# Performance work log

Hardware: AMD Instinct MI355X
Metric: run time of the kernel (lower is better)

## Reference

```python
import jax, jax.numpy as jnp
import numpy as np

# Mamba dims: d_model=1024, expand=2 -> d_inner=2048, d_state=16, d_conv=4, dt_rank=ceil(1024/16)=64
B, L, D = 2, 1024, 1024
DIN, N, R, K = 2048, 16, 64, 4
LN_EPS = 1e-5


def setup_inputs():
    key = jax.random.key(0)
    ks = jax.random.split(key, 12)
    s = lambda fan_in: 1.0 / np.sqrt(fan_in)
    inp = {
        "x": jax.random.normal(ks[0], (B, L, D), jnp.float32),
        "W_in": jax.random.normal(ks[1], (D, 2 * DIN), jnp.float32) * s(D),
        "conv_w": jax.random.normal(ks[2], (DIN, K), jnp.float32) * s(K),
        "conv_b": jax.random.normal(ks[3], (DIN,), jnp.float32) * 0.02,
        "W_x": jax.random.normal(ks[4], (DIN, R + 2 * N), jnp.float32) * s(DIN),
        "W_dt": jax.random.normal(ks[5], (R, DIN), jnp.float32) * s(R),
        # bias chosen so softplus(bias) ~ small positive dt
        "b_dt": jnp.full((DIN,), -4.0, jnp.float32)
        + jax.random.normal(ks[6], (DIN,), jnp.float32) * 0.1,
        # S4D-real init: A = -[1..N] broadcast over channels
        "A_log": jnp.log(jnp.broadcast_to(jnp.arange(1, N + 1, dtype=jnp.float32), (DIN, N))),
        "D_skip": jnp.ones((DIN,), jnp.float32),
        "W_out": jax.random.normal(ks[7], (DIN, D), jnp.float32) * s(DIN),
        "ln_g": jnp.ones((D,), jnp.float32),
        "ln_b": jnp.zeros((D,), jnp.float32),
    }
    return inp


def _silu(x):
    return x * jax.nn.sigmoid(x)


def _mamba_forward(x, W_in, conv_w, conv_b, W_x, W_dt, b_dt, A_log, D_skip, W_out, ln_g, ln_b):
    # in_proj -> (x_in, z), each [B, L, DIN]
    xz = jnp.einsum("bld,de->ble", x, W_in)
    x_in, z = jnp.split(xz, 2, axis=-1)

    # causal depthwise conv1d (kernel K=4) via shifted sums
    xp = jnp.pad(x_in, ((0, 0), (K - 1, 0), (0, 0)))  # [B, L+K-1, DIN]
    x_conv = conv_b
    for k in range(K):
        x_conv = x_conv + xp[:, k : k + L, :] * conv_w[:, k]
    x_conv = _silu(x_conv)  # [B, L, DIN]

    # x_proj -> dt_rank + 2*N
    x_dbl = jnp.einsum("bld,de->ble", x_conv, W_x)
    dt, Bc, Cc = jnp.split(x_dbl, [R, R + N], axis=-1)  # [B,L,R], [B,L,N], [B,L,N]
    delta = jax.nn.softplus(jnp.einsum("blr,rd->bld", dt, W_dt) + b_dt)  # [B,L,DIN]

    A = -jnp.exp(A_log)  # [DIN, N]
    # discretize: deltaA [B,L,DIN,N], deltaB_u [B,L,DIN,N]
    deltaA = jnp.exp(delta[..., None] * A)
    deltaBu = delta[..., None] * Bc[:, :, None, :] * x_conv[..., None]

    # selective scan over time
    def step(h, inp):
        dA, dBu, C_t = inp  # [B,DIN,N], [B,DIN,N], [B,N]
        h = dA * h + dBu
        y_t = jnp.einsum("bdn,bn->bd", h, C_t)
        return h, y_t

    h0 = jnp.zeros((B, DIN, N), jnp.float32)
    xs = (
        jnp.moveaxis(deltaA, 1, 0),
        jnp.moveaxis(deltaBu, 1, 0),
        jnp.moveaxis(Cc, 1, 0),
    )
    _, ys = jax.lax.scan(step, h0, xs)  # ys: [L, B, DIN]
    y = jnp.moveaxis(ys, 0, 1) + x_conv * D_skip  # [B, L, DIN]

    y = y * _silu(z)
    out = jnp.einsum("bld,de->ble", y, W_out)  # [B, L, D]

    # post LayerNorm
    mu = jnp.mean(out, axis=-1, keepdims=True)
    var = jnp.mean(jnp.square(out - mu), axis=-1, keepdims=True)
    return (out - mu) * jax.lax.rsqrt(var + LN_EPS) * ln_g + ln_b


def reference(x, W_in, conv_w, conv_b, W_x, W_dt, b_dt, A_log, D_skip, W_out, ln_g, ln_b):
    return _mamba_forward(x, W_in, conv_w, conv_b, W_x, W_dt, b_dt, A_log, D_skip, W_out, ln_g, ln_b)
```

## Files before the change

kernel.cpp:

```cpp
#include <hip/hip_runtime.h>

#define LSEQ 1024
#define DMODEL 1024
#define DINNER 2048
#define NSTATE 16
#define RRANK 64
#define CHUNK 32
#define NCHUNK 32
#define KSPLIT 8

typedef unsigned short u16;
typedef __attribute__((ext_vector_type(8))) short bf16x8;
typedef __attribute__((ext_vector_type(4))) short bf16x4;
typedef __attribute__((ext_vector_type(4))) float f32x4;

__device__ __forceinline__ float sigmoidf_(float x) {
    return 1.0f / (1.0f + __expf(-x));
}
__device__ __forceinline__ float softplusf_(float x) {
    return (x > 20.0f) ? x : log1pf(__expf(x));
}
__device__ __forceinline__ short f2bf(float f) {
    union { float f; unsigned u; } v; v.f = f;
    unsigned r = v.u + 0x7FFF + ((v.u >> 16) & 1);
    return (short)(r >> 16);
}
__device__ __forceinline__ float bf2f(u16 b) {
    union { unsigned u; float f; } v; v.u = ((unsigned)b) << 16;
    return v.f;
}
__device__ __forceinline__ void async_cp16(const u16* g, u16* l) {
    __builtin_amdgcn_global_load_lds(
        (const __attribute__((address_space(1))) unsigned int*)g,
        (__attribute__((address_space(3))) unsigned int*)l, 16, 0, 0);
}

__global__ __launch_bounds__(256) void cast_bf16_kernel(
    const float* __restrict__ in, u16* __restrict__ out)
{
    const size_t i = ((size_t)blockIdx.x * 256 + threadIdx.x) * 8;
    float4 a = *(const float4*)&in[i];
    float4 b = *(const float4*)&in[i + 4];
    bf16x8 o;
    o[0] = f2bf(a.x); o[1] = f2bf(a.y); o[2] = f2bf(a.z); o[3] = f2bf(a.w);
    o[4] = f2bf(b.x); o[5] = f2bf(b.y); o[6] = f2bf(b.z); o[7] = f2bf(b.w);
    *(bf16x8*)&out[i] = o;
}

__global__ __launch_bounds__(256) void transpose_cast2_kernel(
    const float* __restrict__ in0, u16* __restrict__ out0,
    const float* __restrict__ in1, u16* __restrict__ out1)
{
    __shared__ float t[32][33];
    int bid = blockIdx.x;
    const float* in; u16* out; int R, C, bxi, byi;
    if (bid < 4096) { in = in0; out = out0; R = DMODEL;  C = 2 * DINNER; bxi = bid & 127; byi = bid >> 7; }
    else { bid -= 4096; in = in1; out = out1; R = DINNER; C = DMODEL;    bxi = bid & 31;  byi = bid >> 5; }
    const int bx = bxi * 32, by = byi * 32;
    const int tx = threadIdx.x & 31, ty = threadIdx.x >> 5;
    #pragma unroll
    for (int i = 0; i < 4; ++i)
        t[ty + 8 * i][tx] = in[(size_t)(by + ty + 8 * i) * C + bx + tx];
    __syncthreads();
    #pragma unroll
    for (int i = 0; i < 4; ++i)
        out[(size_t)(bx + ty + 8 * i) * R + by + tx] = (u16)f2bf(t[tx][ty + 8 * i]);
}

template<int BM, int BN, bool BSPLIT>
__global__ __launch_bounds__(256) void mfma_gemm_kernel(
    const u16* __restrict__ A, const u16* __restrict__ Bt,
    float* __restrict__ C0, u16* __restrict__ C1,
    int M, int N, int K, int Nsplit)
{
    constexpr int WMS = BM / 32;
    constexpr int WNS = BN / 32;
    __shared__ u16 lA[BM * 32];
    __shared__ u16 lB[BN * 32];

    const int tid  = threadIdx.x;
    const int lane = tid & 63, wave = tid >> 6;
    const int quad = lane >> 4, l16 = lane & 15;
    const int wm   = (wave >> 1) * (BM / 2);
    const int wn   = (wave & 1) * (BN / 2);
    const int row0 = blockIdx.y * BM;
    const int col0 = blockIdx.x * BN;

    f32x4 acc[WMS][WNS];
    #pragma unroll
    for (int i = 0; i < WMS; ++i)
        #pragma unroll
        for (int j = 0; j < WNS; ++j)
            acc[i][j] = (f32x4){0.f, 0.f, 0.f, 0.f};

    for (int k0 = 0; k0 < K; k0 += 32) {
        #pragma unroll
        for (int t = 0; t < BM / 64; ++t) {
            int c = tid + t * 256;
            int r = c >> 2, kc = c & 3;
            async_cp16(&A[(size_t)(row0 + r) * K + k0 + kc * 8], &lA[c * 8]);
        }
        #pragma unroll
        for (int t = 0; t < BN / 64; ++t) {
            int c = tid + t * 256;
            int r = c >> 2, kc = c & 3;
            async_cp16(&Bt[(size_t)(col0 + r) * K + k0 + kc * 8], &lB[c * 8]);
        }
        __syncthreads();
        bf16x8 af[WMS], bfr[WNS];
        #pragma unroll
        for (int i = 0; i < WMS; ++i)
            af[i] = *(bf16x8*)&lA[(wm + i * 16 + l16) * 32 + quad * 8];
        #pragma unroll
        for (int j = 0; j < WNS; ++j)
            bfr[j] = *(bf16x8*)&lB[(wn + j * 16 + l16) * 32 + quad * 8];
        #pragma unroll
        for (int i = 0; i < WMS; ++i)
            #pragma unroll
            for (int j = 0; j < WNS; ++j)
                acc[i][j] = __builtin_amdgcn_mfma_f32_16x16x32_bf16(
                    af[i], bfr[j], acc[i][j], 0, 0, 0);
        __syncthreads();
    }
    if (!BSPLIT || col0 < Nsplit) {
        const int ldc = BSPLIT ? Nsplit : N;
        #pragma unroll
        for (int i = 0; i < WMS; ++i)
            #pragma unroll
            for (int j = 0; j < WNS; ++j)
                #pragma unroll
                for (int r = 0; r < 4; ++r)
                    C0[(size_t)(row0 + wm + i * 16 + quad * 4 + r) * ldc
                       + col0 + wn + j * 16 + l16] = acc[i][j][r];
    } else {
        const int ldc = N - Nsplit, ccol = col0 - Nsplit;
        #pragma unroll
        for (int i = 0; i < WMS; ++i)
            #pragma unroll
            for (int j = 0; j < WNS; ++j)
                #pragma unroll
                for (int r = 0; r < 4; ++r)
                    C1[(size_t)(row0 + wm + i * 16 + quad * 4 + r) * ldc
                       + ccol + wn + j * 16 + l16] = (u16)f2bf(acc[i][j][r]);
    }
}

__global__ __launch_bounds__(256) void conv_silu_kernel(
    const float* __restrict__ X1, const float* __restrict__ cw,
    const float* __restrict__ cb, u16* __restrict__ xcb)
{
    const int idx = blockIdx.x * 256 + threadIdx.x;
    const int dq  = idx % (DINNER / 4);
    const int bl  = idx / (DINNER / 4);
    const int l   = bl % LSEQ;
    const int d0  = dq * 4;

    const float4* cw4 = (const float4*)cw;
    const float4 W0 = cw4[d0 + 0];
    const float4 W1 = cw4[d0 + 1];
    const float4 W2 = cw4[d0 + 2];
    const float4 W3 = cw4[d0 + 3];
    float4 s = *(const float4*)&cb[d0];

    #pragma unroll
    for (int k = 0; k < 4; ++k) {
        int ls = l + k - 3;
        if (ls >= 0) {
            float4 xv = *(const float4*)&X1[(size_t)(bl + k - 3) * DINNER + d0];
            s.x = fmaf(xv.x, ((const float*)&W0)[k], s.x);
            s.y = fmaf(xv.y, ((const float*)&W1)[k], s.y);
            s.z = fmaf(xv.z, ((const float*)&W2)[k], s.z);
            s.w = fmaf(xv.w, ((const float*)&W3)[k], s.w);
        }
    }
    bf16x4 o;
    o[0] = f2bf(s.x * sigmoidf_(s.x));
    o[1] = f2bf(s.y * sigmoidf_(s.y));
    o[2] = f2bf(s.z * sigmoidf_(s.z));
    o[3] = f2bf(s.w * sigmoidf_(s.w));
    *(bf16x4*)&xcb[(size_t)idx * 4] = o;
}

__global__ __launch_bounds__(256) void xproj_part_kernel(
    const u16* __restrict__ xcb, const float* __restrict__ Wx,
    float* __restrict__ part)
{
    __shared__ float As[32][64 + 4];
    __shared__ float Ws[32][96 + 4];

    const int tid  = threadIdx.x;
    const int tx   = tid % 32;
    const int ty   = tid / 32;
    const int row0 = blockIdx.x * 64;
    const int k0   = blockIdx.y * (DINNER / KSPLIT);

    float acc[8][3];
    #pragma unroll
    for (int i = 0; i < 8; ++i) { acc[i][0] = 0.f; acc[i][1] = 0.f; acc[i][2] = 0.f; }

    for (int kt = 0; kt < DINNER / KSPLIT; kt += 32) {
        const int kb = k0 + kt;
        {
            int m = tid >> 2, kq = tid & 3;
            bf16x8 v = *(const bf16x8*)&xcb[(size_t)(row0 + m) * DINNER + kb + kq * 8];
            #pragma unroll
            for (int j = 0; j < 8; ++j)
                As[kq * 8 + j][m] = bf2f((u16)v[j]);
        }
        #pragma unroll
        for (int i = 0; i < 3; ++i) {
            int lin = tid + i * 256;
            int kk = lin / 24, q = lin % 24;
            *(float4*)&Ws[kk][q * 4] = *(const float4*)&Wx[(size_t)(kb + kk) * 96 + q * 4];
        }
        __syncthreads();
        #pragma unroll 8
        for (int kk = 0; kk < 32; ++kk) {
            float a[8];
            *(float4*)&a[0] = *(const float4*)&As[kk][ty * 8];
            *(float4*)&a[4] = *(const float4*)&As[kk][ty * 8 + 4];
            float b0 = Ws[kk][tx], b1 = Ws[kk][tx + 32], b2 = Ws[kk][tx + 64];
            #pragma unroll
            for (int i = 0; i < 8; ++i) {
                acc[i][0] = fmaf(a[i], b0, acc[i][0]);
                acc[i][1] = fmaf(a[i], b1, acc[i][1]);
                acc[i][2] = fmaf(a[i], b2, acc[i][2]);
            }
        }
        __syncthreads();
    }
    float* po = part + (size_t)blockIdx.y * (2 * LSEQ * 96);
    #pragma unroll
    for (int i = 0; i < 8; ++i) {
        int r = row0 + ty * 8 + i;
        po[(size_t)r * 96 + tx]      = acc[i][0];
        po[(size_t)r * 96 + tx + 32] = acc[i][1];
        po[(size_t)r * 96 + tx + 64] = acc[i][2];
    }
}

__global__ __launch_bounds__(256) void xproj_reduce_kernel(
    const float* __restrict__ part, float* __restrict__ xdbl)
{
    const int idx = blockIdx.x * 256 + threadIdx.x;
    float s = 0.0f;
    #pragma unroll
    for (int k = 0; k < KSPLIT; ++k)
        s += part[(size_t)k * (2 * LSEQ * 96) + idx];
    xdbl[idx] = s;
}

__global__ __launch_bounds__(256) void delta_kernel(
    const float* __restrict__ xdbl, const float* __restrict__ Wdt,
    const float* __restrict__ bdt, u16* __restrict__ deltab)
{
    __shared__ float As[64][64 + 4];
    __shared__ float Ws[64][64 + 4];
    const int tid  = threadIdx.x;
    const int tx   = tid % 16;
    const int ty   = tid / 16;
    const int row0 = blockIdx.y * 64;
    const int col0 = blockIdx.x * 64;

    #pragma unroll
    for (int i = 0; i < 4; ++i) {
        int lin = tid + i * 256;
        int m = lin / 16, kq = lin % 16;
        float4 v = *(const float4*)&xdbl[(size_t)(row0 + m) * 96 + kq * 4];
        As[kq * 4 + 0][m] = v.x;
        As[kq * 4 + 1][m] = v.y;
        As[kq * 4 + 2][m] = v.z;
        As[kq * 4 + 3][m] = v.w;
    }
    #pragma unroll
    for (int i = 0; i < 4; ++i) {
        int lin = tid + i * 256;
        int kk = lin / 16, q = lin % 16;
        *(float4*)&Ws[kk][q * 4] = *(const float4*)&Wdt[(size_t)kk * DINNER + col0 + q * 4];
    }
    __syncthreads();

    float acc[4][4];
    #pragma unroll
    for (int i = 0; i < 4; ++i)
        #pragma unroll
        for (int j = 0; j < 4; ++j) acc[i][j] = 0.0f;

    #pragma unroll 8
    for (int kk = 0; kk < 64; ++kk) {
        float4 a = *(const float4*)&As[kk][ty * 4];
        float4 b = *(const float4*)&Ws[kk][tx * 4];
        const float* ap = (const float*)&a;
        const float* bp = (const float*)&b;
        #pragma unroll
        for (int i = 0; i < 4; ++i)
            #pragma unroll
            for (int j = 0; j < 4; ++j)
                acc[i][j] = fmaf(ap[i], bp[j], acc[i][j]);
    }

    float4 bv = *(const float4*)&bdt[col0 + tx * 4];
    const float* bvp = (const float*)&bv;
    #pragma unroll
    for (int i = 0; i < 4; ++i) {
        bf16x4 o;
        o[0] = f2bf(softplusf_(acc[i][0] + bvp[0]));
        o[1] = f2bf(softplusf_(acc[i][1] + bvp[1]));
        o[2] = f2bf(softplusf_(acc[i][2] + bvp[2]));
        o[3] = f2bf(softplusf_(acc[i][3] + bvp[3]));
        *(bf16x4*)&deltab[(size_t)(row0 + ty * 4 + i) * DINNER + col0 + tx * 4] = o;
    }
}

__global__ __launch_bounds__(256) void scan_part1_kernel(
    const u16* __restrict__ deltab, const u16* __restrict__ xcb,
    const float* __restrict__ xdbl, const float* __restrict__ A_log,
    float* __restrict__ Pbuf, float* __restrict__ Hbuf)
{
    const int d  = blockIdx.x * 256 + threadIdx.x;
    const int b  = blockIdx.y;
    const int ch = blockIdx.z;

    float Aa[NSTATE];
    #pragma unroll
    for (int q = 0; q < 4; ++q) {
        float4 v = *(const float4*)&A_log[(size_t)d * NSTATE + q * 4];
        Aa[q * 4 + 0] = -__expf(v.x);
        Aa[q * 4 + 1] = -__expf(v.y);
        Aa[q * 4 + 2] = -__expf(v.z);
        Aa[q * 4 + 3] = -__expf(v.w);
    }
    float h[NSTATE], P[NSTATE];
    #pragma unroll
    for (int n = 0; n < NSTATE; ++n) { h[n] = 0.0f; P[n] = 1.0f; }

    const size_t row0 = (size_t)b * LSEQ + (size_t)ch * CHUNK;
    #pragma unroll 4
    for (int t = 0; t < CHUNK; ++t) {
        const size_t row = row0 + t;
        float dv  = bf2f(deltab[row * DINNER + d]);
        float xcv = bf2f(xcb[row * DINNER + d]);
        float du  = dv * xcv;
        const float4* br = (const float4*)&xdbl[row * 96 + RRANK];
        float4 B4[4] = { br[0], br[1], br[2], br[3] };
        const float* Bv = (const float*)B4;
        #pragma unroll
        for (int n = 0; n < NSTATE; ++n) {
            float dA = __expf(dv * Aa[n]);
            h[n] = fmaf(dA, h[n], du * Bv[n]);
            P[n] *= dA;
        }
    }
    float* Pp = &Pbuf[(((size_t)ch * 2 + b) * DINNER + d) * NSTATE];
    float* Hp = &Hbuf[(((size_t)ch * 2 + b) * DINNER + d) * NSTATE];
    #pragma unroll
    for (int q = 0; q < 4; ++q) {
        *(float4*)&Pp[q * 4] = *(float4*)&P[q * 4];
        *(float4*)&Hp[q * 4] = *(float4*)&h[q * 4];
    }
}

__global__ __launch_bounds__(256) void scan_combine_kernel(
    const float* __restrict__ Pbuf, const float* __restrict__ Hbuf,
    float* __restrict__ h0buf)
{
    const int idx = blockIdx.x * 256 + threadIdx.x;
    float H = 0.0f;
    #pragma unroll 8
    for (int cch = 0; cch < NCHUNK; ++cch) {
        const size_t g = (size_t)cch * (2 * DINNER * NSTATE) + idx;
        h0buf[g] = H;
        H = fmaf(Pbuf[g], H, Hbuf[g]);
    }
}

__global__ __launch_bounds__(256) void scan_part2_kernel(
    const u16* __restrict__ deltab, const u16* __restrict__ xcb,
    const float* __restrict__ xdbl, const float* __restrict__ h0buf,
    const u16* __restrict__ Zb, u16* __restrict__ yb,
    const float* __restrict__ A_log, const float* __restrict__ Dskip)
{
    const int d  = blockIdx.x * 256 + threadIdx.x;
    const int b  = blockIdx.y;
    const int ch = blockIdx.z;

    float Aa[NSTATE];
    #pragma unroll
    for (int q = 0; q < 4; ++q) {
        float4 v = *(const float4*)&A_log[(size_t)d * NSTATE + q * 4];
        Aa[q * 4 + 0] = -__expf(v.x);
        Aa[q * 4 + 1] = -__expf(v.y);
        Aa[q * 4 + 2] = -__expf(v.z);
        Aa[q * 4 + 3] = -__expf(v.w);
    }
    const float Dd = Dskip[d];

    float h[NSTATE];
    const float* Hp = &h0buf[(((size_t)ch * 2 + b) * DINNER + d) * NSTATE];
    #pragma unroll
    for (int q = 0; q < 4; ++q)
        *(float4*)&h[q * 4] = *(const float4*)&Hp[q * 4];

    const size_t row0 = (size_t)b * LSEQ + (size_t)ch * CHUNK;
    #pragma unroll 2
    for (int t = 0; t < CHUNK; ++t) {
        const size_t row = row0 + t;
        float dv  = bf2f(deltab[row * DINNER + d]);
        float xcv = bf2f(xcb[row * DINNER + d]);
        float du  = dv * xcv;
        const float4* br = (const float4*)&xdbl[row * 96 + RRANK];
        float4 BC[8] = { br[0], br[1], br[2], br[3], br[4], br[5], br[6], br[7] };
        const float* Bv = (const float*)BC;
        const float* Cv = Bv + NSTATE;
        float y = 0.0f;
        #pragma unroll
        for (int n = 0; n < NSTATE; ++n) {
            float dA = __expf(dv * Aa[n]);
            h[n] = fmaf(dA, h[n], du * Bv[n]);
            y = fmaf(h[n], Cv[n], y);
        }
        float zz = bf2f(Zb[row * DINNER + d]);
        float yv = (y + xcv * Dd) * (zz * sigmoidf_(zz));
        yb[row * DINNER + d] = (u16)f2bf(yv);
    }
}

__global__ __launch_bounds__(256) void ln_kernel(
    const float* __restrict__ t, const float* __restrict__ g,
    const float* __restrict__ b, float* __restrict__ out)
{
    const int row = blockIdx.x;
    const int tid = threadIdx.x;
    float4 v = *(const float4*)&t[(size_t)row * DMODEL + tid * 4];
    float s = v.x + v.y + v.z + v.w;
    float q = v.x * v.x + v.y * v.y + v.z * v.z + v.w * v.w;
    #pragma unroll
    for (int m = 1; m < 64; m <<= 1) {
        s += __shfl_xor(s, m, 64);
        q += __shfl_xor(q, m, 64);
    }
    __shared__ float ss[4], qq[4];
    if ((tid & 63) == 0) { ss[tid >> 6] = s; qq[tid >> 6] = q; }
    __syncthreads();
    float S = ss[0] + ss[1] + ss[2] + ss[3];
    float Q = qq[0] + qq[1] + qq[2] + qq[3];
    float mu  = S * (1.0f / DMODEL);
    float var = Q * (1.0f / DMODEL) - mu * mu;
    float rs  = rsqrtf(var + 1e-5f);
    float4 gv = *(const float4*)&g[tid * 4];
    float4 bv = *(const float4*)&b[tid * 4];
    float4 o;
    o.x = (v.x - mu) * rs * gv.x + bv.x;
    o.y = (v.y - mu) * rs * gv.y + bv.y;
    o.z = (v.z - mu) * rs * gv.z + bv.z;
    o.w = (v.w - mu) * rs * gv.w + bv.w;
    *(float4*)&out[(size_t)row * DMODEL + tid * 4] = o;
}

extern "C" void kernel_launch(void* const* d_in, const int* in_sizes, int n_in,
                              void* d_out, int out_size, void* d_ws, size_t ws_size,
                              hipStream_t stream) {
    const float* x      = (const float*)d_in[0];
    const float* W_in   = (const float*)d_in[1];
    const float* conv_w = (const float*)d_in[2];
    const float* conv_b = (const float*)d_in[3];
    const float* W_x    = (const float*)d_in[4];
    const float* W_dt   = (const float*)d_in[5];
    const float* b_dt   = (const float*)d_in[6];
    const float* A_log  = (const float*)d_in[7];
    const float* D_skip = (const float*)d_in[8];
    const float* W_out  = (const float*)d_in[9];
    const float* ln_g   = (const float*)d_in[10];
    const float* ln_b   = (const float*)d_in[11];
    (void)in_sizes; (void)n_in; (void)out_size; (void)ws_size;

    const int M = 2 * LSEQ;

    float* ws    = (float*)d_ws;
    float* X1    = ws;
    float* Zs    = X1    + (size_t)M * DINNER;
    float* xcs   = Zs    + (size_t)M * DINNER;
    float* xdbl  = xcs   + (size_t)M * DINNER;
    float* dls   = xdbl  + (size_t)M * 96;
    float* tmp   = dls   + (size_t)M * DINNER;
    u16*   xb    = (u16*)(tmp + (size_t)M * DMODEL);
    u16*   Wbin  = xb    + (size_t)M * DMODEL;
    u16*   Wbout = Wbin  + (size_t)2 * DINNER * DMODEL;
    u16*   Zb     = (u16*)Zs;
    u16*   xcb    = (u16*)xcs;
    u16*   deltab = (u16*)dls;
    u16*   yb     = (u16*)X1;
    float* Pbuf   = X1 + (size_t)2 * 1024 * 1024;
    float* Hbuf   = (float*)Wbin;
    float* part   = tmp;
    float* h0     = tmp;

    cast_bf16_kernel<<<(M * DMODEL) / (256 * 8), 256, 0, stream>>>(x, xb);
    transpose_cast2_kernel<<<4096 + 2048, 256, 0, stream>>>(W_in, Wbin, W_out, Wbout);

    mfma_gemm_kernel<128, 128, true>
        <<<dim3((2 * DINNER) / 128, M / 128), 256, 0, stream>>>(
            xb, Wbin, X1, Zb, M, 2 * DINNER, DMODEL, DINNER);

    conv_silu_kernel<<<(M * (DINNER / 4)) / 256, 256, 0, stream>>>(
        X1, conv_w, conv_b, xcb);

    xproj_part_kernel<<<dim3(M / 64, KSPLIT), 256, 0, stream>>>(xcb, W_x, part);
    xproj_reduce_kernel<<<(M * 96) / 256, 256, 0, stream>>>(part, xdbl);

    delta_kernel<<<dim3(DINNER / 64, M / 64), 256, 0, stream>>>(
        xdbl, W_dt, b_dt, deltab);

    scan_part1_kernel<<<dim3(DINNER / 256, 2, NCHUNK), 256, 0, stream>>>(
        deltab, xcb, xdbl, A_log, Pbuf, Hbuf);
    scan_combine_kernel<<<(2 * DINNER * NSTATE) / 256, 256, 0, stream>>>(
        Pbuf, Hbuf, h0);
    scan_part2_kernel<<<dim3(DINNER / 256, 2, NCHUNK), 256, 0, stream>>>(
        deltab, xcb, xdbl, h0, Zb, yb, A_log, D_skip);

    mfma_gemm_kernel<64, 64, false>
        <<<dim3(DMODEL / 64, M / 64), 256, 0, stream>>>(
            yb, Wbout, tmp, (u16*)nullptr, M, DMODEL, DINNER, DMODEL);

    ln_kernel<<<M, 256, 0, stream>>>(tmp, ln_g, ln_b, (float*)d_out);
}
```

Baseline: 277.6 us.

## Fuse cast kernels, bf16 in_proj output, split-K out_proj, fold reductions into consumers

Merges the input cast and the two weight transposes into one launch. The in_proj GEMM now writes bf16 for both halves with a BK=64 tile, which halves conv input traffic. The x_proj split-K reduction is folded into the delta kernel, which also emits a compact B/C buffer. The out_proj GEMM moves to 128x128 tiles with 4-way split-K, and its partial sums are reduced inside the LayerNorm kernel. This removes two launches and raises out_proj parallelism, at the cost of more partial-sum traffic and a bf16 rounding of the pre-conv activations.

```diff
diff --git a/kernel.cpp b/kernel.cpp
--- a/kernel.cpp
+++ b/kernel.cpp
@@ -8,6 +8,7 @@
 #define CHUNK 32
 #define NCHUNK 32
 #define KSPLIT 8
+#define MF (1024 * 1024)
 
 typedef unsigned short u16;
 typedef __attribute__((ext_vector_type(8))) short bf16x8;
@@ -35,27 +36,33 @@
         (__attribute__((address_space(3))) unsigned int*)l, 16, 0, 0);
 }
 
-__global__ __launch_bounds__(256) void cast_bf16_kernel(
-    const float* __restrict__ in, u16* __restrict__ out)
-{
-    const size_t i = ((size_t)blockIdx.x * 256 + threadIdx.x) * 8;
-    float4 a = *(const float4*)&in[i];
-    float4 b = *(const float4*)&in[i + 4];
-    bf16x8 o;
-    o[0] = f2bf(a.x); o[1] = f2bf(a.y); o[2] = f2bf(a.z); o[3] = f2bf(a.w);
-    o[4] = f2bf(b.x); o[5] = f2bf(b.y); o[6] = f2bf(b.z); o[7] = f2bf(b.w);
-    *(bf16x8*)&out[i] = o;
-}
-
-__global__ __launch_bounds__(256) void transpose_cast2_kernel(
-    const float* __restrict__ in0, u16* __restrict__ out0,
-    const float* __restrict__ in1, u16* __restrict__ out1)
+__global__ __launch_bounds__(256) void cast_all_kernel(
+    const float* __restrict__ x, u16* __restrict__ xb,
+    const float* __restrict__ Win, u16* __restrict__ Wbin,
+    const float* __restrict__ Wout, u16* __restrict__ Wbout)
 {
     __shared__ float t[32][33];
     int bid = blockIdx.x;
+    if (bid < 1024) {
+        const size_t i = ((size_t)bid * 256 + threadIdx.x) * 8;
+        float4 a = *(const float4*)&x[i];
+        float4 b = *(const float4*)&x[i + 4];
+        bf16x8 o;
+        o[0] = f2bf(a.x); o[1] = f2bf(a.y); o[2] = f2bf(a.z); o[3] = f2bf(a.w);
+        o[4] = f2bf(b.x); o[5] = f2bf(b.y); o[6] = f2bf(b.z); o[7] = f2bf(b.w);
+        *(bf16x8*)&xb[i] = o;
+        return;
+    }
     const float* in; u16* out; int R, C, bxi, byi;
-    if (bid < 4096) { in = in0; out = out0; R = DMODEL;  C = 2 * DINNER; bxi = bid & 127; byi = bid >> 7; }
-    else { bid -= 4096; in = in1; out = out1; R = DINNER; C = DMODEL;    bxi = bid & 31;  byi = bid >> 5; }
+    if (bid < 1024 + 4096) {
+        int tt = bid - 1024;
+        in = Win; out = Wbin; R = DMODEL; C = 2 * DINNER;
+        bxi = tt & 127; byi = tt >> 7;
+    } else {
+        int tt = bid - 5120;
+        in = Wout; out = Wbout; R = DINNER; C = DMODEL;
+        bxi = tt & 31; byi = tt >> 5;
+    }
     const int bx = bxi * 32, by = byi * 32;
     const int tx = threadIdx.x & 31, ty = threadIdx.x >> 5;
     #pragma unroll
@@ -67,16 +74,15 @@
         out[(size_t)(bx + ty + 8 * i) * R + by + tx] = (u16)f2bf(t[tx][ty + 8 * i]);
 }
 
-template<int BM, int BN, bool BSPLIT>
+template<int BM, int BN, int BK, int KSPL, bool BF16OUT>
 __global__ __launch_bounds__(256) void mfma_gemm_kernel(
     const u16* __restrict__ A, const u16* __restrict__ Bt,
-    float* __restrict__ C0, u16* __restrict__ C1,
-    int M, int N, int K, int Nsplit)
+    float* __restrict__ Cf, u16* __restrict__ Cb, int M, int N, int K)
 {
     constexpr int WMS = BM / 32;
     constexpr int WNS = BN / 32;
-    __shared__ u16 lA[BM * 32];
-    __shared__ u16 lB[BN * 32];
+    __shared__ u16 lA[BM * BK];
+    __shared__ u16 lB[BN * BK];
 
     const int tid  = threadIdx.x;
     const int lane = tid & 63, wave = tid >> 6;
@@ -85,6 +91,8 @@
     const int wn   = (wave & 1) * (BN / 2);
     const int row0 = blockIdx.y * BM;
     const int col0 = blockIdx.x * BN;
+    const int Kz   = K / KSPL;
+    const int kbeg = blockIdx.z * Kz;
 
     f32x4 acc[WMS][WNS];
     #pragma unroll
@@ -93,60 +101,62 @@
         for (int j = 0; j < WNS; ++j)
             acc[i][j] = (f32x4){0.f, 0.f, 0.f, 0.f};
 
-    for (int k0 = 0; k0 < K; k0 += 32) {
-        #pragma unroll
-        for (int t = 0; t < BM / 64; ++t) {
+    for (int k0 = kbeg; k0 < kbeg + Kz; k0 += BK) {
+        #pragma unroll
+        for (int t = 0; t < (BM * BK) / 2048; ++t) {
             int c = tid + t * 256;
-            int r = c >> 2, kc = c & 3;
+            int r = c / (BK / 8), kc = c % (BK / 8);
             async_cp16(&A[(size_t)(row0 + r) * K + k0 + kc * 8], &lA[c * 8]);
         }
         #pragma unroll
-        for (int t = 0; t < BN / 64; ++t) {
+        for (int t = 0; t < (BN * BK) / 2048; ++t) {
             int c = tid + t * 256;
-            int r = c >> 2, kc = c & 3;
+            int r = c / (BK / 8), kc = c % (BK / 8);
             async_cp16(&Bt[(size_t)(col0 + r) * K + k0 + kc * 8], &lB[c * 8]);
         }
         __syncthreads();
-        bf16x8 af[WMS], bfr[WNS];
-        #pragma unroll
-        for (int i = 0; i < WMS; ++i)
-            af[i] = *(bf16x8*)&lA[(wm + i * 16 + l16) * 32 + quad * 8];
-        #pragma unroll
-        for (int j = 0; j < WNS; ++j)
-            bfr[j] = *(bf16x8*)&lB[(wn + j * 16 + l16) * 32 + quad * 8];
-        #pragma unroll
-        for (int i = 0; i < WMS; ++i)
+        #pragma unroll
+        for (int ks = 0; ks < BK; ks += 32) {
+            bf16x8 af[WMS], bfr[WNS];
+            #pragma unroll
+            for (int i = 0; i < WMS; ++i)
+                af[i] = *(bf16x8*)&lA[(wm + i * 16 + l16) * BK + ks + quad * 8];
             #pragma unroll
             for (int j = 0; j < WNS; ++j)
-                acc[i][j] = __builtin_amdgcn_mfma_f32_16x16x32_bf16(
-                    af[i], bfr[j], acc[i][j], 0, 0, 0);
+                bfr[j] = *(bf16x8*)&lB[(wn + j * 16 + l16) * BK + ks + quad * 8];
+            #pragma unroll
+            for (int i = 0; i < WMS; ++i)
+                #pragma unroll
+                for (int j = 0; j < WNS; ++j)
+                    acc[i][j] = __builtin_amdgcn_mfma_f32_16x16x32_bf16(
+                        af[i], bfr[j], acc[i][j], 0, 0, 0);
+        }
         __syncthreads();
     }
-    if (!BSPLIT || col0 < Nsplit) {
-        const int ldc = BSPLIT ? Nsplit : N;
+    if (BF16OUT) {
         #pragma unroll
         for (int i = 0; i < WMS; ++i)
             #pragma unroll
             for (int j = 0; j < WNS; ++j)
                 #pragma unroll
                 for (int r = 0; r < 4; ++r)
-                    C0[(size_t)(row0 + wm + i * 16 + quad * 4 + r) * ldc
-                       + col0 + wn + j * 16 + l16] = acc[i][j][r];
+                    Cb[(size_t)(row0 + wm + i * 16 + quad * 4 + r) * N
+                       + col0 + wn + j * 16 + l16] = (u16)f2bf(acc[i][j][r]);
     } else {
-        const int ldc = N - Nsplit, ccol = col0 - Nsplit;
+        float* Cp = Cf + (size_t)blockIdx.z * M * N;
         #pragma unroll
         for (int i = 0; i < WMS; ++i)
             #pragma unroll
             for (int j = 0; j < WNS; ++j)
                 #pragma unroll
                 for (int r = 0; r < 4; ++r)
-                    C1[(size_t)(row0 + wm + i * 16 + quad * 4 + r) * ldc
-                       + ccol + wn + j * 16 + l16] = (u16)f2bf(acc[i][j][r]);
+                    Cp[(size_t)(row0 + wm + i * 16 + quad * 4 + r) * N
+                       + col0 + wn + j * 16 + l16] = acc[i][j][r];
     }
 }
 
 __global__ __launch_bounds__(256) void conv_silu_kernel(
-    const float* __restrict__ X1, const float* __restrict__ cw,
+    const u16* __restrict__ XZb, const float* __restrict__ cw,
     const float* __restrict__ cb, u16* __restrict__ xcb)
 {
     const int idx = blockIdx.x * 256 + threadIdx.x;
@@ -166,11 +176,11 @@
     for (int k = 0; k < 4; ++k) {
         int ls = l + k - 3;
         if (ls >= 0) {
-            float4 xv = *(const float4*)&X1[(size_t)(bl + k - 3) * DINNER + d0];
-            s.x = fmaf(xv.x, ((const float*)&W0)[k], s.x);
-            s.y = fmaf(xv.y, ((const float*)&W1)[k], s.y);
-            s.z = fmaf(xv.z, ((const float*)&W2)[k], s.z);
-            s.w = fmaf(xv.w, ((const float*)&W3)[k], s.w);
+            bf16x4 xv = *(const bf16x4*)&XZb[(size_t)(bl + k - 3) * (2 * DINNER) + d0];
+            s.x = fmaf(bf2f((u16)xv[0]), ((const float*)&W0)[k], s.x);
+            s.y = fmaf(bf2f((u16)xv[1]), ((const float*)&W1)[k], s.y);
+            s.z = fmaf(bf2f((u16)xv[2]), ((const float*)&W2)[k], s.z);
+            s.w = fmaf(bf2f((u16)xv[3]), ((const float*)&W3)[k], s.w);
         }
     }
     bf16x4 o;
@@ -239,20 +249,10 @@
     }
 }
 
-__global__ __launch_bounds__(256) void xproj_reduce_kernel(
-    const float* __restrict__ part, float* __restrict__ xdbl)
-{
-    const int idx = blockIdx.x * 256 + threadIdx.x;
-    float s = 0.0f;
-    #pragma unroll
-    for (int k = 0; k < KSPLIT; ++k)
-        s += part[(size_t)k * (2 * LSEQ * 96) + idx];
-    xdbl[idx] = s;
-}
-
-__global__ __launch_bounds__(256) void delta_kernel(
-    const float* __restrict__ xdbl, const float* __restrict__ Wdt,
-    const float* __restrict__ bdt, u16* __restrict__ deltab)
+__global__ __launch_bounds__(256) void delta_fused_kernel(
+    const float* __restrict__ part, const float* __restrict__ Wdt,
+    const float* __restrict__ bdt, u16* __restrict__ deltab,
+    float* __restrict__ xBC)
 {
     __shared__ float As[64][64 + 4];
     __shared__ float Ws[64][64 + 4];
@@ -266,7 +266,13 @@
     for (int i = 0; i < 4; ++i) {
         int lin = tid + i * 256;
         int m = lin / 16, kq = lin % 16;
-        float4 v = *(const float4*)&xdbl[(size_t)(row0 + m) * 96 + kq * 4];
+        float4 v = {0.f, 0.f, 0.f, 0.f};
+        #pragma unroll
+        for (int s8 = 0; s8 < KSPLIT; ++s8) {
+            float4 p = *(const float4*)&part[(size_t)s8 * (2 * LSEQ * 96)
+                                             + (size_t)(row0 + m) * 96 + kq * 4];
+            v.x += p.x; v.y += p.y; v.z += p.z; v.w += p.w;
+        }
         As[kq * 4 + 0][m] = v.x;
         As[kq * 4 + 1][m] = v.y;
         As[kq * 4 + 2][m] = v.z;
@@ -310,11 +316,25 @@
         o[3] = f2bf(softplusf_(acc[i][3] + bvp[3]));
         *(bf16x4*)&deltab[(size_t)(row0 + ty * 4 + i) * DINNER + col0 + tx * 4] = o;
     }
+
+    if (blockIdx.x == 0) {
+        #pragma unroll
+        for (int i = 0; i < 8; ++i) {
+            int lin = tid + i * 256;
+            int r = lin >> 5, c2 = lin & 31;
+            float s = 0.0f;
+            #pragma unroll
+            for (int s8 = 0; s8 < KSPLIT; ++s8)
+                s += part[(size_t)s8 * (2 * LSEQ * 96)
+                          + (size_t)(row0 + r) * 96 + RRANK + c2];
+            xBC[(size_t)(row0 + r) * 32 + c2] = s;
+        }
+    }
 }
 
 __global__ __launch_bounds__(256) void scan_part1_kernel(
     const u16* __restrict__ deltab, const u16* __restrict__ xcb,
-    const float* __restrict__ xdbl, const float* __restrict__ A_log,
+    const float* __restrict__ xBC, const float* __restrict__ A_log,
     float* __restrict__ Pbuf, float* __restrict__ Hbuf)
 {
     const int d  = blockIdx.x * 256 + threadIdx.x;
@@ -341,7 +361,7 @@
         float dv  = bf2f(deltab[row * DINNER + d]);
         float xcv = bf2f(xcb[row * DINNER + d]);
         float du  = dv * xcv;
-        const float4* br = (const float4*)&xdbl[row * 96 + RRANK];
+        const float4* br = (const float4*)&xBC[row * 32];
         float4 B4[4] = { br[0], br[1], br[2], br[3] };
         const float* Bv = (const float*)B4;
         #pragma unroll
@@ -376,8 +396,8 @@
 
 __global__ __launch_bounds__(256) void scan_part2_kernel(
     const u16* __restrict__ deltab, const u16* __restrict__ xcb,
-    const float* __restrict__ xdbl, const float* __restrict__ h0buf,
-    const u16* __restrict__ Zb, u16* __restrict__ yb,
+    const float* __restrict__ xBC, const float* __restrict__ h0buf,
+    const u16* __restrict__ XZb, u16* __restrict__ yb,
     const float* __restrict__ A_log, const float* __restrict__ Dskip)
 {
     const int d  = blockIdx.x * 256 + threadIdx.x;
@@ -408,7 +428,7 @@
         float dv  = bf2f(deltab[row * DINNER + d]);
         float xcv = bf2f(xcb[row * DINNER + d]);
         float du  = dv * xcv;
-        const float4* br = (const float4*)&xdbl[row * 96 + RRANK];
+        const float4* br = (const float4*)&xBC[row * 32];
         float4 BC[8] = { br[0], br[1], br[2], br[3], br[4], br[5], br[6], br[7] };
         const float* Bv = (const float*)BC;
         const float* Cv = Bv + NSTATE;
@@ -419,19 +439,28 @@
             h[n] = fmaf(dA, h[n], du * Bv[n]);
             y = fmaf(h[n], Cv[n], y);
         }
-        float zz = bf2f(Zb[row * DINNER + d]);
+        float zz = bf2f(XZb[row * (2 * DINNER) + DINNER + d]);
         float yv = (y + xcv * Dd) * (zz * sigmoidf_(zz));
         yb[row * DINNER + d] = (u16)f2bf(yv);
     }
 }
 
-__global__ __launch_bounds__(256) void ln_kernel(
-    const float* __restrict__ t, const float* __restrict__ g,
+__global__ __launch_bounds__(256) void ln4_kernel(
+    const float* __restrict__ p, const float* __restrict__ g,
     const float* __restrict__ b, float* __restrict__ out)
 {
     const int row = blockIdx.x;
     const int tid = threadIdx.x;
-    float4 v = *(const float4*)&t[(size_t)row * DMODEL + tid * 4];
+    const size_t off = (size_t)row * DMODEL + tid * 4;
+    float4 v0 = *(const float4*)&p[off];
+    float4 v1 = *(const float4*)&p[off + 2 * MF];
+    float4 v2 = *(const float4*)&p[off + 4 * (size_t)MF];
+    float4 v3 = *(const float4*)&p[off + 6 * (size_t)MF];
+    float4 v;
+    v.x = (v0.x + v1.x) + (v2.x + v3.x);
+    v.y = (v0.y + v1.y) + (v2.y + v3.y);
+    v.z = (v0.z + v1.z) + (v2.z + v3.z);
+    v.w = (v0.w + v1.w) + (v2.w + v3.w);
     float s = v.x + v.y + v.z + v.w;
     float q = v.x * v.x + v.y * v.y + v.z * v.z + v.w * v.w;
     #pragma unroll
@@ -476,51 +505,46 @@
 
     const int M = 2 * LSEQ;
 
-    float* ws    = (float*)d_ws;
-    float* X1    = ws;
-    float* Zs    = X1    + (size_t)M * DINNER;
-    float* xcs   = Zs    + (size_t)M * DINNER;
-    float* xdbl  = xcs   + (size_t)M * DINNER;
-    float* dls   = xdbl  + (size_t)M * 96;
-    float* tmp   = dls   + (size_t)M * DINNER;
-    u16*   xb    = (u16*)(tmp + (size_t)M * DMODEL);
-    u16*   Wbin  = xb    + (size_t)M * DMODEL;
-    u16*   Wbout = Wbin  + (size_t)2 * DINNER * DMODEL;
-    u16*   Zb     = (u16*)Zs;
-    u16*   xcb    = (u16*)xcs;
-    u16*   deltab = (u16*)dls;
-    u16*   yb     = (u16*)X1;
-    float* Pbuf   = X1 + (size_t)2 * 1024 * 1024;
-    float* Hbuf   = (float*)Wbin;
-    float* part   = tmp;
-    float* h0     = tmp;
-
-    cast_bf16_kernel<<<(M * DMODEL) / (256 * 8), 256, 0, stream>>>(x, xb);
-    transpose_cast2_kernel<<<4096 + 2048, 256, 0, stream>>>(W_in, Wbin, W_out, Wbout);
-
-    mfma_gemm_kernel<128, 128, true>
-        <<<dim3((2 * DINNER) / 128, M / 128), 256, 0, stream>>>(
-            xb, Wbin, X1, Zb, M, 2 * DINNER, DMODEL, DINNER);
+    float* ws     = (float*)d_ws;
+    u16*   XZb    = (u16*)ws;
+    u16*   xcb    = (u16*)(ws + 4 * MF);
+    u16*   deltab = (u16*)(ws + 6 * MF);
+    float* part   = ws + 8 * (size_t)MF;
+    float* Pbuf   = ws + 8 * (size_t)MF;
+    float* Hbuf   = ws + 10 * (size_t)MF;
+    float* h0     = ws + 12 * (size_t)MF;
+    u16*   xb     = (u16*)(ws + 14 * MF);
+    u16*   Wbin   = (u16*)(ws + 15 * MF);
+    u16*   Wbout  = (u16*)(ws + 17 * MF);
+    float* xBC    = ws + 18 * (size_t)MF;
+    u16*   yb     = (u16*)(ws + 15 * MF);
+    float* pout   = ws;
+
+    cast_all_kernel<<<1024 + 4096 + 2048, 256, 0, stream>>>(
+        x, xb, W_in, Wbin, W_out, Wbout);
+
+    mfma_gemm_kernel<128, 128, 64, 1, true>
+        <<<dim3((2 * DINNER) / 128, M / 128, 1), 256, 0, stream>>>(
+            xb, Wbin, nullptr, XZb, M, 2 * DINNER, DMODEL);
 
     conv_silu_kernel<<<(M * (DINNER / 4)) / 256, 256, 0, stream>>>(
-        X1, conv_w, conv_b, xcb);
+        XZb, conv_w, conv_b, xcb);
 
     xproj_part_kernel<<<dim3(M / 64, KSPLIT), 256, 0, stream>>>(xcb, W_x, part);
-    xproj_reduce_kernel<<<(M * 96) / 256, 256, 0, stream>>>(part, xdbl);
-
-    delta_kernel<<<dim3(DINNER / 64, M / 64), 256, 0, stream>>>(
-        xdbl, W_dt, b_dt, deltab);
+
+    delta_fused_kernel<<<dim3(DINNER / 64, M / 64), 256, 0, stream>>>(
+        part, W_dt, b_dt, deltab, xBC);
 
     scan_part1_kernel<<<dim3(DINNER / 256, 2, NCHUNK), 256, 0, stream>>>(
-        deltab, xcb, xdbl, A_log, Pbuf, Hbuf);
+        deltab, xcb, xBC, A_log, Pbuf, Hbuf);
     scan_combine_kernel<<<(2 * DINNER * NSTATE) / 256, 256, 0, stream>>>(
         Pbuf, Hbuf, h0);
     scan_part2_kernel<<<dim3(DINNER / 256, 2, NCHUNK), 256, 0, stream>>>(
-        deltab, xcb, xdbl, h0, Zb, yb, A_log, D_skip);
-
-    mfma_gemm_kernel<64, 64, false>
-        <<<dim3(DMODEL / 64, M / 64), 256, 0, stream>>>(
-            yb, Wbout, tmp, (u16*)nullptr, M, DMODEL, DINNER, DMODEL);
-
-    ln_kernel<<<M, 256, 0, stream>>>(tmp, ln_g, ln_b, (float*)d_out);
-}
+        deltab, xcb, xBC, h0, XZb, yb, A_log, D_skip);
+
+    mfma_gemm_kernel<128, 128, 64, 4, false>
+        <<<dim3(DMODEL / 128, M / 128, 4), 256, 0, stream>>>(
+            yb, Wbout, pout, nullptr, M, DMODEL, DINNER);
+
+    ln4_kernel<<<M, 256, 0, stream>>>(pout, ln_g, ln_b, (float*)d_out);
+}
```

After: 277.7 us. Within noise of the previous version (+0.0%).
